# Kernel tuning notes

Hardware: AMD Instinct MI355X
Metric: run time of the kernel (lower is better)

The kernel has to match this reference:

```python
import jax, jax.numpy as jnp
import numpy as np

B, N, C, K = 16, 2048, 64, 20
RED = 16  # SE reduction


def setup_inputs() -> dict:
    key = jax.random.key(0)
    ks = jax.random.split(key, 8)
    x = jax.random.normal(ks[0], (B * N, C), dtype=jnp.float32)
    batch = jnp.repeat(jnp.arange(B, dtype=jnp.int64), N)
    s1 = 1.0 / np.sqrt(2 * C)
    s2 = 1.0 / np.sqrt(C)
    W1 = jax.random.normal(ks[1], (2 * C, C), dtype=jnp.float32) * s1
    b1 = jnp.zeros((C,), dtype=jnp.float32)
    W2 = jax.random.normal(ks[2], (C, C), dtype=jnp.float32) * s2
    b2 = jnp.zeros((C,), dtype=jnp.float32)
    W3 = jax.random.normal(ks[3], (C, C), dtype=jnp.float32) * s2
    b3 = jnp.zeros((C,), dtype=jnp.float32)
    se_w1 = jax.random.normal(ks[4], (C, C // RED), dtype=jnp.float32) * s2
    se_w2 = jax.random.normal(ks[5], (C // RED, C), dtype=jnp.float32) * (1.0 / np.sqrt(C // RED))
    sa_w = jax.random.normal(ks[6], (1, 2, 7), dtype=jnp.float32) * (1.0 / np.sqrt(14))
    return {"x": x, "batch": batch, "batch_size": B, "W1": W1, "b1": b1,
            "W2": W2, "b2": b2, "W3": W3, "b3": b3,
            "se_w1": se_w1, "se_w2": se_w2, "sa_w": sa_w}


def _forward(x, batch_size, W1, b1, W2, b2, W3, b3, se_w1, se_w2, sa_w):
    n = x.shape[0] // batch_size
    xb = x.reshape(batch_size, n, -1)              # [B,N,C]
    # --- dynamic kNN graph (self point included, as in PyG knn) ---
    sq = jnp.sum(xb * xb, axis=-1)                 # [B,N]
    d = sq[:, :, None] + sq[:, None, :] - 2.0 * jnp.einsum('bic,bjc->bij', xb, xb)
    _, idx = jax.lax.top_k(-d, K)                  # [B,N,K] nearest (incl self)
    xj = jax.vmap(lambda pts, ids: pts[ids])(xb, idx)   # [B,N,K,C]
    xi = xb[:, :, None, :]
    edge = jnp.concatenate([jnp.broadcast_to(xi, xj.shape), xj - xi], axis=-1)  # [B,N,K,2C]
    # --- shared edge MLP ---
    h = jax.nn.relu(edge @ W1 + b1)
    h = jax.nn.relu(h @ W2 + b2)
    h = h @ W3 + b3                                 # [B,N,K,C]
    agg = jnp.max(h, axis=2)                        # [B,N,C] max-aggregate
    # --- SE channel attention (pool over points) ---
    s = jnp.mean(agg, axis=1)                       # [B,C]
    y = jax.nn.sigmoid(jax.nn.relu(s @ se_w1) @ se_w2)  # [B,C]
    x_se = agg * y[:, None, :]
    # --- spatial attention (pool over channels, conv1d k=7) ---
    avg_out = jnp.mean(x_se, axis=2)                # [B,N]
    max_out = jnp.max(x_se, axis=2)                 # [B,N]
    ycat = jnp.stack([avg_out, max_out], axis=1)    # [B,2,N]
    att = jax.lax.conv_general_dilated(ycat, sa_w, (1,), [(3, 3)],
                                       dimension_numbers=('NCH', 'OIH', 'NCH'))  # [B,1,N]
    att = jax.nn.sigmoid(att)
    x_att = x_se * att.transpose(0, 2, 1)           # [B,N,C]
    # --- residual (in_channels == out_channels) ---
    out = x_att + xb
    return out.reshape(batch_size * n, -1)


def reference(x, batch, batch_size, W1, b1, W2, b2, W3, b3, se_w1, se_w2, sa_w):
    return _forward(x, batch_size, W1, b1, W2, b2, W3, b3, se_w1, se_w2, sa_w)
```

## Files before the change

kernel.cpp:

```cpp
#include <hip/hip_runtime.h>

typedef unsigned int uint32;
typedef unsigned long long uint64;
typedef unsigned short ushortT;
typedef __attribute__((ext_vector_type(8))) short short8;
typedef __attribute__((ext_vector_type(4))) short short4v;
typedef __attribute__((ext_vector_type(4))) float floatx4;

#define DEV static __device__ __forceinline__

#define NN 2048
#define CC 64
#define KK 20

DEV float bf2f(ushortT h) {
  union { uint32 u; float f; } c; c.u = ((uint32)h) << 16; return c.f;
}
DEV ushortT f2bf(float f) {
  union { float f; uint32 u; } c; c.f = f;
  uint32 r = c.u + 0x7FFFu + ((c.u >> 16) & 1u);
  return (ushortT)(r >> 16);
}
DEV void split2(float v, ushortT& h, ushortT& l) {
  h = f2bf(v);
  l = f2bf(v - bf2f(h));
}
DEV uint32 fmap(float f) {
  uint32 u = __float_as_uint(f);
  return (u & 0x80000000u) ? ~u : (u | 0x80000000u);
}
DEV float funmap(uint32 m) {
  uint32 u = (m & 0x80000000u) ? (m ^ 0x80000000u) : ~m;
  return __uint_as_float(u);
}
DEV short8 ld8(const ushortT* p) {
  short4v a = *(const short4v*)p;
  short4v b = *(const short4v*)(p + 4);
  short8 r;
  r[0] = a.x; r[1] = a.y; r[2] = a.z; r[3] = a.w;
  r[4] = b.x; r[5] = b.y; r[6] = b.z; r[7] = b.w;
  return r;
}

__global__ void k_sq(const float* __restrict__ x, float* __restrict__ sq,
                     ushortT* __restrict__ xbf) {
  int p = blockIdx.x * 256 + threadIdx.x;
  const float4* row = (const float4*)(x + (size_t)p * CC);
  ushortT* orow = xbf + (size_t)p * CC;
  float s = 0.f;
#pragma unroll
  for (int q = 0; q < 16; ++q) {
    float4 v = row[q];
    s += v.x * v.x + v.y * v.y + v.z * v.z + v.w * v.w;
    short4v h;
    h.x = (short)f2bf(v.x); h.y = (short)f2bf(v.y);
    h.z = (short)f2bf(v.z); h.w = (short)f2bf(v.w);
    *(short4v*)(orow + q * 4) = h;
  }
  sq[p] = s;
}

__global__ void k_wconv(const float* __restrict__ w1, const float* __restrict__ w2,
                        const float* __restrict__ w3, ushortT* __restrict__ wbf) {
  int t = threadIdx.x;
  for (int e = t; e < 4096; e += 256) {
    int n = e >> 6, k = e & 63;
    wbf[e]         = f2bf(w1[k * 64 + n]);
    wbf[4096 + e]  = f2bf(w1[(64 + k) * 64 + n]);
    wbf[8192 + e]  = f2bf(w2[k * 64 + n]);
    wbf[12288 + e] = f2bf(w3[k * 64 + n]);
  }
}

__launch_bounds__(256, 4)
__global__ void k_knn(const ushortT* __restrict__ xbf, const float* __restrict__ sq,
                      ushortT* __restrict__ cand) {
  const int b  = blockIdx.y;
  const int i0 = blockIdx.x * 32;
  const int t  = threadIdx.x;
  const int l  = t & 63, wv = t >> 6;
  const int la = l & 15, quad = l >> 4;
  const int pp = t >> 2, ss = t & 3;

  __shared__ __align__(16) char sm[35968];
  ushortT (*sXj)[72]    = (ushortT(*)[72])(sm);
  uint32  (*sCand)[130] = (uint32(*)[130])(sm + 18432);
  uint32*  sTau         = (uint32*)(sm + 35072);
  uint32*  sCnt         = (uint32*)(sm + 35200);
  float*   sSqi         = (float*)(sm + 35328);
  float*   sSqj         = (float*)(sm + 35456);

  const ushortT* xbb = xbf + ((size_t)b * NN) * CC;

  const int mw  = wv & 1;
  const int nt0 = (wv >> 1) * 4;

  short8 afrag[2];
  {
    const ushortT* rowp = xbb + (size_t)(i0 + mw * 16 + la) * CC;
#pragma unroll
    for (int ks = 0; ks < 2; ++ks)
      afrag[ks] = *(const short8*)(rowp + ks * 32 + quad * 8);
  }
  if (t < 32) sSqi[t] = sq[b * NN + i0 + t];

  {
    int r = t >> 1, co = (t & 1) * 32;
    const ushortT* src = xbb + (size_t)r * CC + co;
#pragma unroll
    for (int i = 0; i < 4; ++i)
      *(uint4*)&sXj[r][co + i * 8] = *(const uint4*)(src + i * 8);
  }
  if (t < 128) sSqj[t] = sq[b * NN + t];

  uint32 lst[KK];
#pragma unroll
  for (int s = 0; s < KK; ++s) lst[s] = 0xFFFFFFFFu;

  __syncthreads();

  float sqa[4];
  {
    float4 v = *(const float4*)&sSqi[mw * 16 + quad * 4];
    sqa[0] = v.x; sqa[1] = v.y; sqa[2] = v.z; sqa[3] = v.w;
  }

  for (int jt = 0; jt < 16; ++jt) {
    const int j0 = jt * 128;

    floatx4 acc[4];
#pragma unroll
    for (int n = 0; n < 4; ++n) acc[n] = (floatx4){0.f, 0.f, 0.f, 0.f};

#pragma unroll
    for (int ks = 0; ks < 2; ++ks) {
      int kof = ks * 32 + quad * 8;
#pragma unroll
      for (int n = 0; n < 4; ++n) {
        short8 bv = *(const short8*)&sXj[(nt0 + n) * 16 + la][kof];
        acc[n] = __builtin_amdgcn_mfma_f32_16x16x32_bf16(afrag[ks], bv, acc[n], 0, 0, 0);
      }
    }

    if (jt == 0) {
#pragma unroll
      for (int n = 0; n < 4; ++n) {
        int jl = (nt0 + n) * 16 + la;
        float dj = sSqj[jl];
        uint32 jg = (uint32)(j0 + jl);
#pragma unroll
        for (int rg = 0; rg < 4; ++rg) {
          int il = mw * 16 + quad * 4 + rg;
          float d = fmaxf(sqa[rg] + dj - 2.0f * acc[n][rg], 0.f);
          sCand[il][jl] = (__float_as_uint(d) & 0xFFFFF800u) | jg;
        }
      }
    } else {
      uint32 tv[4];
      {
        uint4 u = *(const uint4*)&sTau[mw * 16 + quad * 4];
        tv[0] = u.x; tv[1] = u.y; tv[2] = u.z; tv[3] = u.w;
      }
#pragma unroll
      for (int n = 0; n < 4; ++n) {
        int jl = (nt0 + n) * 16 + la;
        float dj = sSqj[jl];
        uint32 jg = (uint32)(j0 + jl);
#pragma unroll
        for (int rg = 0; rg < 4; ++rg) {
          int il = mw * 16 + quad * 4 + rg;
          float d = fmaxf(sqa[rg] + dj - 2.0f * acc[n][rg], 0.f);
          uint32 key = (__float_as_uint(d) & 0xFFFFF800u) | jg;
          if (key < tv[rg]) {
            uint32 slot = atomicAdd(&sCnt[il], 1u);
            sCand[il][slot] = key;
          }
        }
      }
    }
    __syncthreads();

    if (t < 128) {
      int cnt = (jt == 0) ? 128 : (int)sCnt[pp];
      for (int q = ss; q < cnt; q += 4) {
        uint32 cur = sCand[pp][q];
#pragma unroll
        for (int s = 0; s < KK; ++s) {
          uint32 lo = min(lst[s], cur);
          cur = max(lst[s], cur);
          lst[s] = lo;
        }
      }
      uint32 m19 = lst[KK - 1];
      m19 = min(m19, (uint32)__shfl_xor((int)m19, 1));
      m19 = min(m19, (uint32)__shfl_xor((int)m19, 2));
      if (ss == 0) { sTau[pp] = m19; sCnt[pp] = 0u; }
    }

    if (jt < 15) {
      const int jn = (jt + 1) * 128;
      int r = t >> 1, co = (t & 1) * 32;
      const ushortT* src = xbb + (size_t)(jn + r) * CC + co;
#pragma unroll
      for (int i = 0; i < 4; ++i)
        *(uint4*)&sXj[r][co + i * 8] = *(const uint4*)(src + i * 8);
      if (t < 128) sSqj[t] = sq[b * NN + jn + t];
    }
    __syncthreads();
  }

  if (t < 128) {
    size_t base = ((size_t)(b * NN + i0 + pp)) * 80 + ss * KK;
#pragma unroll
    for (int s = 0; s < KK; ++s) cand[base + s] = (ushortT)(lst[s] & 2047u);
  }
}

__launch_bounds__(256, 4)
__global__ void k_rerank(const float* __restrict__ x, const ushortT* __restrict__ cand,
                         int* __restrict__ idxout) {
  const int b  = blockIdx.y;
  const int i0 = blockIdx.x * 16;
  const int t  = threadIdx.x;
  const int grp = t >> 4, lg = t & 15;

  __shared__ double sK[16][81];

  const float* xb = x + ((size_t)b * NN) * CC;
  const int p = i0 + grp;
  float4 vi = ((const float4*)(xb + (size_t)p * CC))[lg];
  size_t cb = ((size_t)(b * NN + p)) * 80;

  const bool hi8 = (lg & 8) != 0;
  const bool hi4 = (lg & 4) != 0;
  const bool hi2 = (lg & 2) != 0;
  const int  uslot = ((lg >> 1) & 1) | (((lg >> 2) & 1) << 1) | (((lg >> 3) & 1) << 2);

  for (int q0 = 0; q0 < 80; q0 += 8) {
    int jj0 = (int)cand[cb + q0 + 0], jj1 = (int)cand[cb + q0 + 1];
    int jj2 = (int)cand[cb + q0 + 2], jj3 = (int)cand[cb + q0 + 3];
    int jj4 = (int)cand[cb + q0 + 4], jj5 = (int)cand[cb + q0 + 5];
    int jj6 = (int)cand[cb + q0 + 6], jj7 = (int)cand[cb + q0 + 7];

#define DISTQ(JJ, DD)                                                        \
    double DD;                                                               \
    {                                                                        \
      float4 vj = ((const float4*)(xb + (size_t)(JJ) * CC))[lg];             \
      double e0 = (double)vi.x - (double)vj.x;                               \
      double e1 = (double)vi.y - (double)vj.y;                               \
      double e2 = (double)vi.z - (double)vj.z;                               \
      double e3 = (double)vi.w - (double)vj.w;                               \
      DD = e0 * e0 + e1 * e1 + e2 * e2 + e3 * e3;                            \
    }
    DISTQ(jj0, dd0) DISTQ(jj1, dd1) DISTQ(jj2, dd2) DISTQ(jj3, dd3)
    DISTQ(jj4, dd4) DISTQ(jj5, dd5) DISTQ(jj6, dd6) DISTQ(jj7, dd7)
#undef DISTQ

    double m0 = hi8 ? dd4 : dd0, s0 = hi8 ? dd0 : dd4;
    double m1 = hi8 ? dd5 : dd1, s1 = hi8 ? dd1 : dd5;
    double m2 = hi8 ? dd6 : dd2, s2 = hi8 ? dd2 : dd6;
    double m3 = hi8 ? dd7 : dd3, s3 = hi8 ? dd3 : dd7;
    double r40 = m0 + __shfl_xor(s0, 8, 16);
    double r41 = m1 + __shfl_xor(s1, 8, 16);
    double r42 = m2 + __shfl_xor(s2, 8, 16);
    double r43 = m3 + __shfl_xor(s3, 8, 16);
    int j40 = hi8 ? jj4 : jj0, j41 = hi8 ? jj5 : jj1;
    int j42 = hi8 ? jj6 : jj2, j43 = hi8 ? jj7 : jj3;

    double n0 = hi4 ? r42 : r40, t0 = hi4 ? r40 : r42;
    double n1 = hi4 ? r43 : r41, t1 = hi4 ? r41 : r43;
    double r20 = n0 + __shfl_xor(t0, 4, 16);
    double r21 = n1 + __shfl_xor(t1, 4, 16);
    int j20 = hi4 ? j42 : j40, j21 = hi4 ? j43 : j41;

    double p0 = hi2 ? r21 : r20, u0 = hi2 ? r20 : r21;
    double r1 = p0 + __shfl_xor(u0, 2, 16);
    int j1 = hi2 ? j21 : j20;

    r1 += __shfl_xor(r1, 1, 16);

    if ((lg & 1) == 0) {
      uint64 bits = (uint64)__double_as_longlong(r1);
      sK[grp][q0 + uslot] = __longlong_as_double((bits & ~2047ULL) | (uint64)j1);
    }
  }
  __syncthreads();

  double k5[5];
#pragma unroll
  for (int s = 0; s < 5; ++s) k5[s] = sK[grp][lg + 16 * s];

  const double DINF = __longlong_as_double(0x7FF0000000000000LL);
  size_t obase = ((size_t)(b * NN + p)) * KK;
  for (int r = 0; r < KK; ++r) {
    double lm = fmin(fmin(fmin(k5[0], k5[1]), fmin(k5[2], k5[3])), k5[4]);
#pragma unroll
    for (int off = 8; off > 0; off >>= 1)
      lm = fmin(lm, __shfl_xor(lm, off, 16));
#pragma unroll
    for (int s = 0; s < 5; ++s) k5[s] = (k5[s] == lm) ? DINF : k5[s];
    if (lg == (r & 15))
      idxout[obase + r] = (int)((uint64)__double_as_longlong(lm) & 2047ULL);
  }
}

__launch_bounds__(256, 4)
__global__ void k_mlp(const float* __restrict__ x, const ushortT* __restrict__ xbf,
                      const int* __restrict__ idx, const ushortT* __restrict__ wbf,
                      const float* __restrict__ b1, const float* __restrict__ b2,
                      const float* __restrict__ b3, float* __restrict__ agg) {
  const int b  = blockIdx.y;
  const int i0 = blockIdx.x * 4;
  const int t  = threadIdx.x;
  const int l  = t & 63, wv = t >> 6;
  const int la = l & 15, quad = l >> 4;

  __shared__ __align__(16) char sm[35008];
  ushortT (*sDH)[68]  = (ushortT(*)[68])(sm + 0);
  ushortT (*sDL)[68]  = (ushortT(*)[68])(sm + 10880);
  ushortT (*sH1)[68]  = (ushortT(*)[68])(sm + 21760);
  float   (*sPre)[64] = (float(*)[64])(sm + 32640);
  uint32*  sAgg       = (uint32*)(sm + 33664);
  int*     sJ         = (int*)(sm + 34688);
  ushortT (*sH2)[68]  = sDH;

  const int c = wv * 16 + la;
  const ushortT* w1aT = wbf;
  const ushortT* w1bT = wbf + 4096;
  const ushortT* w2T  = wbf + 8192;
  const ushortT* w3T  = wbf + 12288;

  if (t < 80) {
    int p = t / 20, kk = t - p * 20;
    int v = idx[((size_t)(b * NN + i0 + p)) * KK + kk];
    v = v < 0 ? 0 : (v > (NN - 1) ? (NN - 1) : v);
    sJ[t] = v;
  }
  sAgg[t] = 0u;

  float b2c = b2[c], b3c = b3[c];

  {
    float b1c = b1[c];
    floatx4 ap = (floatx4){b1c, b1c, b1c, b1c};
#pragma unroll
    for (int ks = 0; ks < 2; ++ks) {
      short8 av = *(const short8*)(xbf + (size_t)(b * NN + i0 + (la & 3)) * CC + ks * 32 + quad * 8);
      short8 bv = *(const short8*)(w1aT + c * 64 + ks * 32 + quad * 8);
      ap = __builtin_amdgcn_mfma_f32_16x16x32_bf16(av, bv, ap, 0, 0, 0);
    }
    if (quad == 0) {
#pragma unroll
      for (int rg = 0; rg < 4; ++rg) sPre[rg][c] = ap[rg];
    }
  }
  __syncthreads();

  const float* xb = x + ((size_t)b * NN) * CC;
  for (int e = t; e < 1280; e += 256) {
    int r = e >> 4, c4g = e & 15, c4 = c4g * 4;
    int p = r / 20;
    float4 vi = ((const float4*)(xb + (size_t)(i0 + p) * CC))[c4g];
    float4 vj = ((const float4*)(xb + (size_t)sJ[r] * CC))[c4g];
    short4v dh, dl;
    ushortT hh, ll;
    split2(vj.x - vi.x, hh, ll); dh.x = (short)hh; dl.x = (short)ll;
    split2(vj.y - vi.y, hh, ll); dh.y = (short)hh; dl.y = (short)ll;
    split2(vj.z - vi.z, hh, ll); dh.z = (short)hh; dl.z = (short)ll;
    split2(vj.w - vi.w, hh, ll); dh.w = (short)hh; dl.w = (short)ll;
    *(short4v*)&sDH[r][c4] = dh;
    *(short4v*)&sDL[r][c4] = dl;
  }
  __syncthreads();

  {
    short8 bB[2];
#pragma unroll
    for (int ks = 0; ks < 2; ++ks)
      bB[ks] = *(const short8*)(w1bT + c * 64 + ks * 32 + quad * 8);
#pragma unroll
    for (int m5 = 0; m5 < 5; ++m5) {
      floatx4 a;
#pragma unroll
      for (int rg = 0; rg < 4; ++rg) {
        int r = m5 * 16 + quad * 4 + rg;
        a[rg] = sPre[r / 20][c];
      }
#pragma unroll
      for (int ks = 0; ks < 2; ++ks) {
        int kof = ks * 32 + quad * 8;
        short8 aDH = ld8(&sDH[m5 * 16 + la][kof]);
        short8 aDL = ld8(&sDL[m5 * 16 + la][kof]);
        a = __builtin_amdgcn_mfma_f32_16x16x32_bf16(aDH, bB[ks], a, 0, 0, 0);
        a = __builtin_amdgcn_mfma_f32_16x16x32_bf16(aDL, bB[ks], a, 0, 0, 0);
      }
#pragma unroll
      for (int rg = 0; rg < 4; ++rg) {
        int r = m5 * 16 + quad * 4 + rg;
        sH1[r][c] = f2bf(fmaxf(a[rg], 0.f));
      }
    }
  }
  __syncthreads();

  {
    short8 bf[2];
#pragma unroll
    for (int ks = 0; ks < 2; ++ks)
      bf[ks] = *(const short8*)(w2T + c * 64 + ks * 32 + quad * 8);
#pragma unroll
    for (int m5 = 0; m5 < 5; ++m5) {
      floatx4 a = (floatx4){b2c, b2c, b2c, b2c};
#pragma unroll
      for (int ks = 0; ks < 2; ++ks) {
        short8 aH = ld8(&sH1[m5 * 16 + la][ks * 32 + quad * 8]);
        a = __builtin_amdgcn_mfma_f32_16x16x32_bf16(aH, bf[ks], a, 0, 0, 0);
      }
#pragma unroll
      for (int rg = 0; rg < 4; ++rg) {
        int r = m5 * 16 + quad * 4 + rg;
        sH2[r][c] = f2bf(fmaxf(a[rg], 0.f));
      }
    }
  }
  __syncthreads();

  {
    short8 bf[2];
#pragma unroll
    for (int ks = 0; ks < 2; ++ks)
      bf[ks] = *(const short8*)(w3T + c * 64 + ks * 32 + quad * 8);
#pragma unroll
    for (int m5 = 0; m5 < 5; ++m5) {
      floatx4 a = (floatx4){b3c, b3c, b3c, b3c};
#pragma unroll
      for (int ks = 0; ks < 2; ++ks) {
        short8 aH = ld8(&sH2[m5 * 16 + la][ks * 32 + quad * 8]);
        a = __builtin_amdgcn_mfma_f32_16x16x32_bf16(aH, bf[ks], a, 0, 0, 0);
      }
#pragma unroll
      for (int rg = 0; rg < 4; ++rg) {
        int r = m5 * 16 + quad * 4 + rg;
        int p = r / 20;
        atomicMax(&sAgg[p * 64 + c], fmap(a[rg]));
      }
    }
  }
  __syncthreads();

  {
    int p = t >> 6, cc = t & 63;
    agg[((size_t)(b * NN + i0 + p)) * CC + cc] = funmap(sAgg[t]);
  }
}

__global__ void k_se(const float* __restrict__ agg, const float* __restrict__ sew1,
                     const float* __restrict__ sew2, float* __restrict__ y) {
  int b = blockIdx.x, t = threadIdx.x;
  int c = t & 63, q = t >> 6;
  __shared__ float part[4][64];
  __shared__ float sv[64];
  __shared__ float hid[4];
  const float* ab = agg + ((size_t)b * NN) * CC;
  float s = 0.f;
  for (int n = q * 512; n < q * 512 + 512; ++n) s += ab[(size_t)n * CC + c];
  part[q][c] = s;
  __syncthreads();
  if (t < 64) sv[t] = (part[0][t] + part[1][t] + part[2][t] + part[3][t]) * (1.f / 2048.f);
  __syncthreads();
  if (t < 4) {
    float a = 0.f;
    for (int cc = 0; cc < 64; ++cc) a += sv[cc] * sew1[cc * 4 + t];
    hid[t] = fmaxf(a, 0.f);
  }
  __syncthreads();
  if (t < 64) {
    float a = 0.f;
#pragma unroll
    for (int h = 0; h < 4; ++h) a += hid[h] * sew2[h * 64 + t];
    y[b * 64 + t] = 1.f / (1.f + expf(-a));
  }
}

__global__ void k_stats(const float* __restrict__ agg, const float* __restrict__ y,
                        float* __restrict__ ycat) {
  int t = threadIdx.x;
  int gid = blockIdx.x * 4 + (t >> 6);
  int l = t & 63;
  int b = gid >> 11, i = gid & 2047;
  float v = agg[(size_t)gid * CC + l] * y[b * 64 + l];
  float s = v, mx = v;
#pragma unroll
  for (int off = 32; off > 0; off >>= 1) {
    s += __shfl_xor(s, off);
    mx = fmaxf(mx, __shfl_xor(mx, off));
  }
  if (l == 0) {
    ycat[b * 2 * NN + i] = s * (1.f / 64.f);
    ycat[b * 2 * NN + NN + i] = mx;
  }
}

__global__ void k_final(const float* __restrict__ agg, const float* __restrict__ y,
                        const float* __restrict__ ycat, const float* __restrict__ saw,
                        const float* __restrict__ x, float* __restrict__ out) {
  int e = blockIdx.x * 256 + threadIdx.x;
  int ifl = e >> 6, c = e & 63;
  int b = ifl >> 11, i = ifl & 2047;
  float a = 0.f;
#pragma unroll
  for (int w = 0; w < 7; ++w) {
    int ii = i + w - 3;
    if (ii >= 0 && ii < NN) {
      a += ycat[b * 2 * NN + ii] * saw[w];
      a += ycat[b * 2 * NN + NN + ii] * saw[7 + w];
    }
  }
  float att = 1.f / (1.f + expf(-a));
  out[e] = agg[(size_t)ifl * CC + c] * y[b * 64 + c] * att + x[(size_t)e];
}

extern "C" void kernel_launch(void* const* d_in, const int* in_sizes, int n_in,
                              void* d_out, int out_size, void* d_ws, size_t ws_size,
                              hipStream_t stream) {
  const float* x    = (const float*)d_in[0];
  const float* w1   = (const float*)d_in[3];
  const float* b1   = (const float*)d_in[4];
  const float* w2   = (const float*)d_in[5];
  const float* b2   = (const float*)d_in[6];
  const float* w3   = (const float*)d_in[7];
  const float* b3   = (const float*)d_in[8];
  const float* sew1 = (const float*)d_in[9];
  const float* sew2 = (const float*)d_in[10];
  const float* saw  = (const float*)d_in[11];
  float* out = (float*)d_out;

  char* ws = (char*)d_ws;
  float*   sq   = (float*)  (ws);
  int*     idx  = (int*)    (ws + 131072);
  ushortT* cand = (ushortT*)(ws + 2752512);
  float*   agg  = (float*)  (ws + 2752512);
  float*   y    = (float*)  (ws + 11141120);
  float*   ycat = (float*)  (ws + 11145216);
  ushortT* wbf  = (ushortT*)(ws + 11407360);

  ushortT* xbf = (ushortT*)d_out;

  k_wconv <<<1,              256, 0, stream>>>(w1, w2, w3, wbf);
  k_sq    <<<128,            256, 0, stream>>>(x, sq, xbf);
  k_knn   <<<dim3(64, 16),   256, 0, stream>>>(xbf, sq, cand);
  k_rerank<<<dim3(128, 16),  256, 0, stream>>>(x, cand, idx);
  k_mlp   <<<dim3(512, 16),  256, 0, stream>>>(x, xbf, idx, wbf, b1, b2, b3, agg);
  k_se    <<<16,             256, 0, stream>>>(agg, sew1, sew2, y);
  k_stats <<<8192,           256, 0, stream>>>(agg, y, ycat);
  k_final <<<8192,           256, 0, stream>>>(agg, y, ycat, saw, x, out);
}
```

Before: 315.4 us.

## Halve kNN column tile for occupancy and split SE pooling across blocks

The kNN kernel now processes 64 candidate columns per iteration instead of 128. This halves its shared memory so that 8 blocks can be resident per CU, at the cost of twice as many iterations and barriers. The SE channel mean was a 16-block serial reduction over 2048 rows per batch. It is now split into a 256-block partial-sum kernel followed by a small combine kernel. That adds one launch but raises parallelism in the pooling step. Partial sums reuse the idx workspace region, which is dead by that point.

Result: slower. 362.0 us (+14.8%).

```diff
diff --git a/kernel.cpp b/kernel.cpp
--- a/kernel.cpp
+++ b/kernel.cpp
@@ -72,7 +72,7 @@
   }
 }
 
-__launch_bounds__(256, 4)
+__launch_bounds__(256, 8)
 __global__ void k_knn(const ushortT* __restrict__ xbf, const float* __restrict__ sq,
                       ushortT* __restrict__ cand) {
   const int b  = blockIdx.y;
@@ -82,18 +82,18 @@
   const int la = l & 15, quad = l >> 4;
   const int pp = t >> 2, ss = t & 3;
 
-  __shared__ __align__(16) char sm[35968];
-  ushortT (*sXj)[72]    = (ushortT(*)[72])(sm);
-  uint32  (*sCand)[130] = (uint32(*)[130])(sm + 18432);
-  uint32*  sTau         = (uint32*)(sm + 35072);
-  uint32*  sCnt         = (uint32*)(sm + 35200);
-  float*   sSqi         = (float*)(sm + 35328);
-  float*   sSqj         = (float*)(sm + 35456);
+  __shared__ __align__(16) char sm[18304];
+  ushortT (*sXj)[72]   = (ushortT(*)[72])(sm);
+  uint32  (*sCand)[66] = (uint32(*)[66])(sm + 9216);
+  uint32*  sTau        = (uint32*)(sm + 17664);
+  uint32*  sCnt        = (uint32*)(sm + 17792);
+  float*   sSqi        = (float*)(sm + 17920);
+  float*   sSqj        = (float*)(sm + 18048);
 
   const ushortT* xbb = xbf + ((size_t)b * NN) * CC;
 
-  const int mw  = wv & 1;
-  const int nt0 = (wv >> 1) * 4;
+  const int mw = wv & 1;
+  const int ng = wv >> 1;
 
   short8 afrag[2];
   {
@@ -105,13 +105,12 @@
   if (t < 32) sSqi[t] = sq[b * NN + i0 + t];
 
   {
-    int r = t >> 1, co = (t & 1) * 32;
+    int r = t >> 2, co = (t & 3) * 16;
     const ushortT* src = xbb + (size_t)r * CC + co;
-#pragma unroll
-    for (int i = 0; i < 4; ++i)
-      *(uint4*)&sXj[r][co + i * 8] = *(const uint4*)(src + i * 8);
-  }
-  if (t < 128) sSqj[t] = sq[b * NN + t];
+    *(uint4*)&sXj[r][co]     = *(const uint4*)(src);
+    *(uint4*)&sXj[r][co + 8] = *(const uint4*)(src + 8);
+  }
+  if (t < 64) sSqj[t] = sq[b * NN + t];
 
   uint32 lst[KK];
 #pragma unroll
@@ -125,27 +124,27 @@
     sqa[0] = v.x; sqa[1] = v.y; sqa[2] = v.z; sqa[3] = v.w;
   }
 
-  for (int jt = 0; jt < 16; ++jt) {
-    const int j0 = jt * 128;
-
-    floatx4 acc[4];
-#pragma unroll
-    for (int n = 0; n < 4; ++n) acc[n] = (floatx4){0.f, 0.f, 0.f, 0.f};
+  for (int jt = 0; jt < 32; ++jt) {
+    const int j0 = jt * 64;
+
+    floatx4 acc[2];
+#pragma unroll
+    for (int n = 0; n < 2; ++n) acc[n] = (floatx4){0.f, 0.f, 0.f, 0.f};
 
 #pragma unroll
     for (int ks = 0; ks < 2; ++ks) {
       int kof = ks * 32 + quad * 8;
 #pragma unroll
-      for (int n = 0; n < 4; ++n) {
-        short8 bv = *(const short8*)&sXj[(nt0 + n) * 16 + la][kof];
+      for (int n = 0; n < 2; ++n) {
+        short8 bv = *(const short8*)&sXj[(ng * 2 + n) * 16 + la][kof];
         acc[n] = __builtin_amdgcn_mfma_f32_16x16x32_bf16(afrag[ks], bv, acc[n], 0, 0, 0);
       }
     }
 
     if (jt == 0) {
 #pragma unroll
-      for (int n = 0; n < 4; ++n) {
-        int jl = (nt0 + n) * 16 + la;
+      for (int n = 0; n < 2; ++n) {
+        int jl = (ng * 2 + n) * 16 + la;
         float dj = sSqj[jl];
         uint32 jg = (uint32)(j0 + jl);
 #pragma unroll
@@ -162,8 +161,8 @@
         tv[0] = u.x; tv[1] = u.y; tv[2] = u.z; tv[3] = u.w;
       }
 #pragma unroll
-      for (int n = 0; n < 4; ++n) {
-        int jl = (nt0 + n) * 16 + la;
+      for (int n = 0; n < 2; ++n) {
+        int jl = (ng * 2 + n) * 16 + la;
         float dj = sSqj[jl];
         uint32 jg = (uint32)(j0 + jl);
 #pragma unroll
@@ -181,7 +180,7 @@
     __syncthreads();
 
     if (t < 128) {
-      int cnt = (jt == 0) ? 128 : (int)sCnt[pp];
+      int cnt = (jt == 0) ? 64 : (int)sCnt[pp];
       for (int q = ss; q < cnt; q += 4) {
         uint32 cur = sCand[pp][q];
 #pragma unroll
@@ -197,14 +196,13 @@
       if (ss == 0) { sTau[pp] = m19; sCnt[pp] = 0u; }
     }
 
-    if (jt < 15) {
-      const int jn = (jt + 1) * 128;
-      int r = t >> 1, co = (t & 1) * 32;
+    if (jt < 31) {
+      const int jn = (jt + 1) * 64;
+      int r = t >> 2, co = (t & 3) * 16;
       const ushortT* src = xbb + (size_t)(jn + r) * CC + co;
-#pragma unroll
-      for (int i = 0; i < 4; ++i)
-        *(uint4*)&sXj[r][co + i * 8] = *(const uint4*)(src + i * 8);
-      if (t < 128) sSqj[t] = sq[b * NN + jn + t];
+      *(uint4*)&sXj[r][co]     = *(const uint4*)(src);
+      *(uint4*)&sXj[r][co + 8] = *(const uint4*)(src + 8);
+      if (t < 64) sSqj[t] = sq[b * NN + jn + t];
     }
     __syncthreads();
   }
@@ -454,19 +452,31 @@
   }
 }
 
-__global__ void k_se(const float* __restrict__ agg, const float* __restrict__ sew1,
-                     const float* __restrict__ sew2, float* __restrict__ y) {
+__global__ void k_se1(const float* __restrict__ agg, float* __restrict__ part) {
+  int b = blockIdx.x >> 4, ch = blockIdx.x & 15;
+  int t = threadIdx.x;
+  int c = t & 63, q = t >> 6;
+  __shared__ float red[4][64];
+  const float* ab = agg + ((size_t)(b * NN) + ch * 128) * CC;
+  float s = 0.f;
+  for (int r = q * 32; r < q * 32 + 32; ++r) s += ab[(size_t)r * CC + c];
+  red[q][c] = s;
+  __syncthreads();
+  if (t < 64)
+    part[blockIdx.x * 64 + t] = (red[0][t] + red[1][t]) + (red[2][t] + red[3][t]);
+}
+
+__global__ void k_se2(const float* __restrict__ part, const float* __restrict__ sew1,
+                      const float* __restrict__ sew2, float* __restrict__ y) {
   int b = blockIdx.x, t = threadIdx.x;
-  int c = t & 63, q = t >> 6;
-  __shared__ float part[4][64];
   __shared__ float sv[64];
   __shared__ float hid[4];
-  const float* ab = agg + ((size_t)b * NN) * CC;
-  float s = 0.f;
-  for (int n = q * 512; n < q * 512 + 512; ++n) s += ab[(size_t)n * CC + c];
-  part[q][c] = s;
-  __syncthreads();
-  if (t < 64) sv[t] = (part[0][t] + part[1][t] + part[2][t] + part[3][t]) * (1.f / 2048.f);
+  {
+    float s = 0.f;
+#pragma unroll
+    for (int k = 0; k < 16; ++k) s += part[(b * 16 + k) * 64 + t];
+    sv[t] = s * (1.f / 2048.f);
+  }
   __syncthreads();
   if (t < 4) {
     float a = 0.f;
@@ -474,7 +484,7 @@
     hid[t] = fmaxf(a, 0.f);
   }
   __syncthreads();
-  if (t < 64) {
+  {
     float a = 0.f;
 #pragma unroll
     for (int h = 0; h < 4; ++h) a += hid[h] * sew2[h * 64 + t];
@@ -538,6 +548,7 @@
   char* ws = (char*)d_ws;
   float*   sq   = (float*)  (ws);
   int*     idx  = (int*)    (ws + 131072);
+  float*   part = (float*)  (ws + 131072);
   ushortT* cand = (ushortT*)(ws + 2752512);
   float*   agg  = (float*)  (ws + 2752512);
   float*   y    = (float*)  (ws + 11141120);
@@ -551,7 +562,8 @@
   k_knn   <<<dim3(64, 16),   256, 0, stream>>>(xbf, sq, cand);
   k_rerank<<<dim3(128, 16),  256, 0, stream>>>(x, cand, idx);
   k_mlp   <<<dim3(512, 16),  256, 0, stream>>>(x, xbf, idx, wbf, b1, b2, b3, agg);
-  k_se    <<<16,             256, 0, stream>>>(agg, sew1, sew2, y);
+  k_se1   <<<256,            256, 0, stream>>>(agg, part);
+  k_se2   <<<16,             64,  0, stream>>>(part, sew1, sew2, y);
   k_stats <<<8192,           256, 0, stream>>>(agg, y, ycat);
   k_final <<<8192,           256, 0, stream>>>(agg, y, ycat, saw, x, out);
 }
```
